# Optimization experiments

Measured on AMD Instinct MI355X. Metric: run time of the kernel, lower is better.

## Reference

```python
import jax, jax.numpy as jnp
import numpy as np

NUM_QUBITS = 4
NUM_LAYERS = 3


def _ry(state, theta, wire):
    # state: (N,2,2,2,2) real amplitudes; RY(theta) on `wire` (angle scalar or (N,))
    st = jnp.moveaxis(state, wire + 1, -1)
    c = jnp.cos(theta * 0.5)
    s = jnp.sin(theta * 0.5)
    if jnp.ndim(c) == 1:  # per-sample angle -> broadcast over remaining qubit axes
        shape = (c.shape[0],) + (1,) * (st.ndim - 2)
        c = c.reshape(shape)
        s = s.reshape(shape)
    s0, s1 = st[..., 0], st[..., 1]
    new = jnp.stack([c * s0 - s * s1, s * s0 + c * s1], axis=-1)
    return jnp.moveaxis(new, -1, wire + 1)


def _cnot(state, control, target):
    st = jnp.moveaxis(state, (control + 1, target + 1), (-2, -1))
    new = jnp.stack([st[..., 0, :], st[..., 1, ::-1]], axis=-2)
    return jnp.moveaxis(new, (-2, -1), (control + 1, target + 1))


def _circuit(angles, params):
    # angles: (N,4) input rotations; params: (L,4,1) shared variational angles
    N = angles.shape[0]
    state = jnp.zeros((N, 2, 2, 2, 2), angles.dtype).at[:, 0, 0, 0, 0].set(1.0)
    for q in range(NUM_QUBITS):
        state = _ry(state, angles[:, q], q)
    for l in range(NUM_LAYERS):
        for q in range(NUM_QUBITS):
            state = _ry(state, params[l, q, 0], q)
        for q in range(NUM_QUBITS - 1):
            state = _cnot(state, q, q + 1)
    probs = state * state  # amplitudes are real (only RY/CNOT)
    meas = []
    for w in range(NUM_QUBITS):
        axes = tuple(a for a in range(1, NUM_QUBITS + 1) if a != w + 1)
        p = probs.sum(axes)  # (N,2)
        meas.append(p[:, 0] - p[:, 1])  # <Z_w>
    return jnp.stack(meas, axis=-1)  # (N,4)


def setup_inputs() -> dict:
    key = jax.random.key(0)
    k1, k2, k3, k4, k5 = jax.random.split(key, 5)
    B = 8192
    return {
        "x": jax.random.uniform(k1, (B, 1, 28, 28), dtype=jnp.float32),
        "params": jax.random.normal(k2, (NUM_LAYERS, NUM_QUBITS, 1), dtype=jnp.float32),
        "res_w": jax.random.normal(k3, (4, 1, 1, 1), dtype=jnp.float32),
        "cls_w": jax.random.normal(k4, (10, 784), dtype=jnp.float32) * 0.03,
        "cls_b": jax.random.normal(k5, (10,), dtype=jnp.float32) * 0.03,
    }


def reference(x, params, res_w, cls_w, cls_b):
    B = x.shape[0]
    img = x.reshape(B, 28, 28)
    # extract 2x2 patches, element order (r,c),(r,c+1),(r+1,c),(r+1,c+1)
    patches = img.reshape(B, 14, 2, 14, 2).transpose(0, 1, 3, 2, 4).reshape(B, 196, 4)
    # per-patch-index min/max over batch and the 4 elements (matches patch.min()/max())
    mn = patches.min(axis=(0, 2), keepdims=True)
    mx = patches.max(axis=(0, 2), keepdims=True)
    ang = (patches - mn) / (mx - mn + 1e-8) * jnp.pi
    meas = _circuit(ang.reshape(B * 196, 4), params)  # (B*196, 4)
    out = meas.reshape(B, 196 * 4).reshape(B, 4, 14, 14)  # matches torch.cat(...).view
    # res_conv: 1x1 conv, stride 2, no bias -> strided pixel scaled per out-channel
    res = img[:, ::2, ::2][:, None, :, :] * res_w.reshape(1, 4, 1, 1)
    out = out + res
    logits = out.reshape(B, -1) @ cls_w.T + cls_b
    return jax.nn.log_softmax(logits, axis=-1)
```

## Files before the change

### kernel.cpp

```cpp
#include <hip/hip_runtime.h>
#include <math.h>

#define NP 196
#define PI_F 3.14159265358979323846f

__device__ __forceinline__ unsigned fkey(float f) {
  unsigned u = __float_as_uint(f);
  return u ^ ((unsigned)((int)u >> 31) | 0x80000000u);
}
__device__ __forceinline__ float funkey(unsigned k) {
  unsigned u = (k & 0x80000000u) ? (k ^ 0x80000000u) : ~k;
  return __uint_as_float(u);
}

__global__ void __launch_bounds__(256) precompute_kernel(
    const float* __restrict__ params, const float* __restrict__ res_w,
    const float* __restrict__ cls_w, float* __restrict__ U,
    float* __restrict__ W2, unsigned* __restrict__ mn,
    unsigned* __restrict__ mx) {
  const int tid = threadIdx.x;
  if (tid < NP) {
    mn[tid] = 0xFFFFFFFFu;
    mx[tid] = 0u;
  }
  if (tid < 16) {
    float cp[12], sp[12];
#pragma unroll
    for (int l = 0; l < 12; ++l) __sincosf(0.5f * params[l], &sp[l], &cp[l]);
    float st[16];
#pragma unroll
    for (int i = 0; i < 16; ++i) st[i] = 0.f;
    st[tid] = 1.f;
#pragma unroll
    for (int l = 0; l < 3; ++l) {
#pragma unroll
      for (int q = 0; q < 4; ++q) {
        const float cq = cp[l * 4 + q], sq = sp[l * 4 + q];
        const int m = 8 >> q;
#pragma unroll
        for (int idx = 0; idx < 16; ++idx) {
          if (idx & m) continue;
          float v0 = st[idx], v1 = st[idx | m];
          st[idx] = cq * v0 - sq * v1;
          st[idx | m] = sq * v0 + cq * v1;
        }
      }
#pragma unroll
      for (int q = 0; q < 3; ++q) {
        const int mc = 8 >> q, mt = 4 >> q;
#pragma unroll
        for (int idx = 0; idx < 16; ++idx) {
          if ((idx & mc) && !(idx & mt)) {
            float t0 = st[idx];
            st[idx] = st[idx | mt];
            st[idx | mt] = t0;
          }
        }
      }
    }
#pragma unroll
    for (int i = 0; i < 16; ++i) U[i * 16 + tid] = st[i];
  }
  for (int t = tid; t < 10 * NP; t += 256) {
    int k = t / NP, p = t - k * NP;
    float s = 0.f;
#pragma unroll
    for (int c = 0; c < 4; ++c) s += res_w[c] * cls_w[k * 784 + c * NP + p];
    W2[t] = s;
  }
}

__global__ void __launch_bounds__(512) minmax_kernel(
    const float* __restrict__ x, unsigned* __restrict__ mn,
    unsigned* __restrict__ mx, int imgs, int B) {
  __shared__ unsigned skmin[392], skmax[392];
  const int t = threadIdx.x;
  const int img0 = blockIdx.x * imgs;
  if (t < 392) {
    const int r = t / 14, j = t - r * 14;
    const float* base = x + (size_t)img0 * 784 + r * 28 + 2 * j;
    float lmn = 3.4e38f, lmx = -3.4e38f;
    const int nimg = (img0 + imgs <= B) ? imgs : (B - img0);
#pragma unroll 4
    for (int m = 0; m < nimg; ++m) {
      float2 v = *(const float2*)(base + (size_t)m * 784);
      lmn = fminf(lmn, fminf(v.x, v.y));
      lmx = fmaxf(lmx, fmaxf(v.x, v.y));
    }
    skmin[t] = fkey(lmn);
    skmax[t] = fkey(lmx);
  }
  __syncthreads();
  if (t < NP) {
    const int i = t / 14, j = t - i * 14;
    const int f0 = (2 * i) * 14 + j, f1 = f0 + 14;
    unsigned kmn = skmin[f0] < skmin[f1] ? skmin[f0] : skmin[f1];
    unsigned kmx = skmax[f0] > skmax[f1] ? skmax[f0] : skmax[f1];
    atomicMin(&mn[t], kmn);
    atomicMax(&mx[t], kmx);
  }
}

__global__ void __launch_bounds__(256) fused_kernel(
    const float* __restrict__ x, const unsigned* __restrict__ mnk,
    const unsigned* __restrict__ mxk, const float* __restrict__ U,
    const float* __restrict__ W2, const float* __restrict__ cls_w,
    const float* __restrict__ cls_b, float* __restrict__ out) {
  __shared__ float lmeas[784];
  __shared__ float respix[NP];
  __shared__ float partial[4][10];

  const int t = threadIdx.x;
  const int b = blockIdx.x;

  if (t < NP) {
    const int p = t;
    const int i = p / 14, j = p - i * 14;
    const float* px = x + (size_t)b * 784 + (2 * i) * 28 + 2 * j;
    const float2 r0 = *(const float2*)px;
    const float2 r1 = *(const float2*)(px + 28);

    const float mnv = funkey(mnk[p]);
    const float mxv = funkey(mxk[p]);
    const float sc = (0.5f * PI_F) / (mxv - mnv + 1e-8f);

    float cc[4], ss[4];
    __sincosf((r0.x - mnv) * sc, &ss[0], &cc[0]);
    __sincosf((r0.y - mnv) * sc, &ss[1], &cc[1]);
    __sincosf((r1.x - mnv) * sc, &ss[2], &cc[2]);
    __sincosf((r1.y - mnv) * sc, &ss[3], &cc[3]);

    float st0[16];
    {
      const float A[4] = {cc[0] * cc[1], cc[0] * ss[1], ss[0] * cc[1], ss[0] * ss[1]};
      const float Bq[4] = {cc[2] * cc[3], cc[2] * ss[3], ss[2] * cc[3], ss[2] * ss[3]};
#pragma unroll
      for (int idx = 0; idx < 16; ++idx) st0[idx] = A[idx >> 2] * Bq[idx & 3];
    }

    float sq[16];
#pragma unroll
    for (int i2 = 0; i2 < 16; ++i2) {
      float f = 0.f;
#pragma unroll
      for (int jx = 0; jx < 16; ++jx) f = fmaf(U[i2 * 16 + jx], st0[jx], f);
      sq[i2] = f * f;
    }
    float a[8], z3 = 0.f;
#pragma unroll
    for (int k = 0; k < 8; ++k) {
      a[k] = sq[2 * k] + sq[2 * k + 1];
      z3 += sq[2 * k] - sq[2 * k + 1];
    }
    float bb[4], z2 = 0.f;
#pragma unroll
    for (int k = 0; k < 4; ++k) {
      bb[k] = a[2 * k] + a[2 * k + 1];
      z2 += a[2 * k] - a[2 * k + 1];
    }
    const float e0 = bb[0] + bb[1], e1 = bb[2] + bb[3];
    const float z1 = (bb[0] - bb[1]) + (bb[2] - bb[3]);
    const float z0 = e0 - e1;

    lmeas[4 * p + 0] = z0;
    lmeas[4 * p + 1] = z1;
    lmeas[4 * p + 2] = z2;
    lmeas[4 * p + 3] = z3;
    respix[p] = r0.x;
  }
  __syncthreads();

  float acc[10];
#pragma unroll
  for (int k = 0; k < 10; ++k) acc[k] = 0.f;

  for (int f = t; f < 784; f += 256) {
    const float v = lmeas[f];
#pragma unroll
    for (int k = 0; k < 10; ++k) acc[k] = fmaf(v, cls_w[k * 784 + f], acc[k]);
  }
  if (t < NP) {
    const float v = respix[t];
#pragma unroll
    for (int k = 0; k < 10; ++k) acc[k] = fmaf(v, W2[k * NP + t], acc[k]);
  }

  const int lane = t & 63, wv = t >> 6;
#pragma unroll
  for (int k = 0; k < 10; ++k) {
    float v = acc[k];
#pragma unroll
    for (int off = 32; off > 0; off >>= 1) v += __shfl_down(v, off, 64);
    if (lane == 0) partial[wv][k] = v;
  }
  __syncthreads();

  if (t == 0) {
    float lg[10];
#pragma unroll
    for (int k = 0; k < 10; ++k)
      lg[k] = partial[0][k] + partial[1][k] + partial[2][k] + partial[3][k] + cls_b[k];
    float m = lg[0];
#pragma unroll
    for (int k = 1; k < 10; ++k) m = fmaxf(m, lg[k]);
    float s = 0.f;
#pragma unroll
    for (int k = 0; k < 10; ++k) s += __expf(lg[k] - m);
    const float lse = m + __logf(s);
#pragma unroll
    for (int k = 0; k < 10; ++k) out[(size_t)b * 10 + k] = lg[k] - lse;
  }
}

extern "C" void kernel_launch(void* const* d_in, const int* in_sizes, int n_in,
                              void* d_out, int out_size, void* d_ws, size_t ws_size,
                              hipStream_t stream) {
  const float* x      = (const float*)d_in[0];
  const float* params = (const float*)d_in[1];
  const float* res_w  = (const float*)d_in[2];
  const float* cls_w  = (const float*)d_in[3];
  const float* cls_b  = (const float*)d_in[4];
  float* out = (float*)d_out;
  const int B = in_sizes[0] / 784;

  unsigned* mn = (unsigned*)d_ws;
  unsigned* mx = mn + NP;
  float* U  = (float*)(mx + NP);
  float* W2 = U + 256;

  precompute_kernel<<<1, 256, 0, stream>>>(params, res_w, cls_w, U, W2, mn, mx);

  const int imgs = 16;
  const int nblk1 = (B + imgs - 1) / imgs;
  minmax_kernel<<<nblk1, 512, 0, stream>>>(x, mn, mx, imgs, B);

  fused_kernel<<<B, 256, 0, stream>>>(x, mn, mx, U, W2, cls_w, cls_b, out);
}
```

Before: 129.9 us.

## Fuse classifier dot into per-patch threads, drop shared staging and barrier

```diff
diff --git a/kernel.cpp b/kernel.cpp
--- a/kernel.cpp
+++ b/kernel.cpp
@@ -79,16 +79,26 @@
   if (t < 392) {
     const int r = t / 14, j = t - r * 14;
     const float* base = x + (size_t)img0 * 784 + r * 28 + 2 * j;
-    float lmn = 3.4e38f, lmx = -3.4e38f;
     const int nimg = (img0 + imgs <= B) ? imgs : (B - img0);
+    float lmn0 = 3.4e38f, lmn1 = 3.4e38f;
+    float lmx0 = -3.4e38f, lmx1 = -3.4e38f;
+    int m = 0;
 #pragma unroll 4
-    for (int m = 0; m < nimg; ++m) {
-      float2 v = *(const float2*)(base + (size_t)m * 784);
-      lmn = fminf(lmn, fminf(v.x, v.y));
-      lmx = fmaxf(lmx, fmaxf(v.x, v.y));
-    }
-    skmin[t] = fkey(lmn);
-    skmax[t] = fkey(lmx);
+    for (; m + 1 < nimg; m += 2) {
+      float2 v0 = *(const float2*)(base + (size_t)m * 784);
+      float2 v1 = *(const float2*)(base + (size_t)(m + 1) * 784);
+      lmn0 = fminf(lmn0, fminf(v0.x, v0.y));
+      lmx0 = fmaxf(lmx0, fmaxf(v0.x, v0.y));
+      lmn1 = fminf(lmn1, fminf(v1.x, v1.y));
+      lmx1 = fmaxf(lmx1, fmaxf(v1.x, v1.y));
+    }
+    if (m < nimg) {
+      float2 v0 = *(const float2*)(base + (size_t)m * 784);
+      lmn0 = fminf(lmn0, fminf(v0.x, v0.y));
+      lmx0 = fmaxf(lmx0, fmaxf(v0.x, v0.y));
+    }
+    skmin[t] = fkey(fminf(lmn0, lmn1));
+    skmax[t] = fkey(fmaxf(lmx0, lmx1));
   }
   __syncthreads();
   if (t < NP) {
@@ -106,12 +116,14 @@
     const unsigned* __restrict__ mxk, const float* __restrict__ U,
     const float* __restrict__ W2, const float* __restrict__ cls_w,
     const float* __restrict__ cls_b, float* __restrict__ out) {
-  __shared__ float lmeas[784];
-  __shared__ float respix[NP];
   __shared__ float partial[4][10];
 
   const int t = threadIdx.x;
   const int b = blockIdx.x;
+
+  float acc[10];
+#pragma unroll
+  for (int k = 0; k < 10; ++k) acc[k] = 0.f;
 
   if (t < NP) {
     const int p = t;
@@ -138,60 +150,48 @@
       for (int idx = 0; idx < 16; ++idx) st0[idx] = A[idx >> 2] * Bq[idx & 3];
     }
 
-    float sq[16];
-#pragma unroll
-    for (int i2 = 0; i2 < 16; ++i2) {
-      float f = 0.f;
-#pragma unroll
-      for (int jx = 0; jx < 16; ++jx) f = fmaf(U[i2 * 16 + jx], st0[jx], f);
-      sq[i2] = f * f;
-    }
-    float a[8], z3 = 0.f;
+    float a8[8], z3 = 0.f;
 #pragma unroll
     for (int k = 0; k < 8; ++k) {
-      a[k] = sq[2 * k] + sq[2 * k + 1];
-      z3 += sq[2 * k] - sq[2 * k + 1];
+      float f0 = 0.f, f1 = 0.f;
+#pragma unroll
+      for (int jx = 0; jx < 16; ++jx) {
+        f0 = fmaf(U[(2 * k) * 16 + jx], st0[jx], f0);
+        f1 = fmaf(U[(2 * k + 1) * 16 + jx], st0[jx], f1);
+      }
+      const float s0 = f0 * f0, s1 = f1 * f1;
+      a8[k] = s0 + s1;
+      z3 += s0 - s1;
     }
     float bb[4], z2 = 0.f;
 #pragma unroll
     for (int k = 0; k < 4; ++k) {
-      bb[k] = a[2 * k] + a[2 * k + 1];
-      z2 += a[2 * k] - a[2 * k + 1];
+      bb[k] = a8[2 * k] + a8[2 * k + 1];
+      z2 += a8[2 * k] - a8[2 * k + 1];
     }
     const float e0 = bb[0] + bb[1], e1 = bb[2] + bb[3];
     const float z1 = (bb[0] - bb[1]) + (bb[2] - bb[3]);
     const float z0 = e0 - e1;
-
-    lmeas[4 * p + 0] = z0;
-    lmeas[4 * p + 1] = z1;
-    lmeas[4 * p + 2] = z2;
-    lmeas[4 * p + 3] = z3;
-    respix[p] = r0.x;
-  }
-  __syncthreads();
-
-  float acc[10];
-#pragma unroll
-  for (int k = 0; k < 10; ++k) acc[k] = 0.f;
-
-  for (int f = t; f < 784; f += 256) {
-    const float v = lmeas[f];
-#pragma unroll
-    for (int k = 0; k < 10; ++k) acc[k] = fmaf(v, cls_w[k * 784 + f], acc[k]);
-  }
-  if (t < NP) {
-    const float v = respix[t];
-#pragma unroll
-    for (int k = 0; k < 10; ++k) acc[k] = fmaf(v, W2[k * NP + t], acc[k]);
+    const float v = r0.x;
+
+#pragma unroll
+    for (int k = 0; k < 10; ++k) {
+      const float4 w4 = *(const float4*)(cls_w + k * 784 + 4 * p);
+      float a = z0 * w4.x;
+      a = fmaf(z1, w4.y, a);
+      a = fmaf(z2, w4.z, a);
+      a = fmaf(z3, w4.w, a);
+      acc[k] = fmaf(v, W2[k * NP + p], a);
+    }
   }
 
   const int lane = t & 63, wv = t >> 6;
 #pragma unroll
   for (int k = 0; k < 10; ++k) {
-    float v = acc[k];
-#pragma unroll
-    for (int off = 32; off > 0; off >>= 1) v += __shfl_down(v, off, 64);
-    if (lane == 0) partial[wv][k] = v;
+    float a = acc[k];
+#pragma unroll
+    for (int off = 32; off > 0; off >>= 1) a += __shfl_down(a, off, 64);
+    if (lane == 0) partial[wv][k] = a;
   }
   __syncthreads();
 
```

Result: faster. 127.1 us (-2.2%).
